# Kernel optimization log

Hardware: AMD Instinct MI355X
Metric: run time of the kernel (lower is better)

Reference implementation:

```python
import jax, jax.numpy as jnp
import numpy as np

B, H, W, C = 8, 64, 64, 256
CK = C // 8  # key/query dim of conv_f / conv_g


def setup_inputs() -> dict:
    key = jax.random.key(0)
    ks = jax.random.split(key, 10)
    s = lambda fan_in: 1.0 / np.sqrt(fan_in)
    return {
        "x": jax.random.normal(ks[0], (B, H, W, C), dtype=jnp.float32),
        "Wf": jax.random.normal(ks[1], (C, CK), dtype=jnp.float32) * s(C),
        "bf": jnp.zeros((CK,), dtype=jnp.float32),
        "Wg": jax.random.normal(ks[2], (C, CK), dtype=jnp.float32) * s(C),
        "bg": jnp.zeros((CK,), dtype=jnp.float32),
        "Wh": jax.random.normal(ks[3], (C, C), dtype=jnp.float32) * s(C),
        "bh": jnp.zeros((C,), dtype=jnp.float32),
        "Wo": jax.random.normal(ks[4], (C, C), dtype=jnp.float32) * s(C),
        "bo": jnp.zeros((C,), dtype=jnp.float32),
        # original init is zeros; use a random scalar so output/grads are nontrivial
        "gamma": jax.random.normal(ks[5], (1,), dtype=jnp.float32),
    }


def reference(x, Wf, bf, Wg, bg, Wh, bh, Wo, bo, gamma):
    b, h, w, c = x.shape
    n = h * w
    xf = x.reshape(b, n, c)                       # flatten spatial: [B, N, C]
    # 1x1 convs == per-pixel matmuls
    f = xf @ Wf + bf                              # [B, N, C//8]
    g = xf @ Wg + bg                              # [B, N, C//8]
    hh = xf @ Wh + bh                             # [B, N, C]
    # scores[b, i, j] = <g_i, f_j>; softmax over j (keys)
    scores = jnp.einsum("bnd,bmd->bnm", g, f)     # [B, N, N]
    attn = jax.nn.softmax(scores, axis=-1)
    o = jnp.einsum("bnm,bmc->bnc", attn, hh)      # [B, N, C]
    o = o @ Wo + bo                               # conv_o (1x1)
    out = gamma * o + xf                          # gamma residual
    return out.reshape(b, h, w, c)
```

## Files before the change

### kernel.cpp

```cpp
#include <hip/hip_runtime.h>
#include <hip/hip_fp16.h>
#include <hip/hip_bf16.h>

constexpr int BB  = 8;
constexpr int NN  = 4096;
constexpr int CC  = 256;
constexpr int CKK = 32;

typedef __attribute__((ext_vector_type(8))) short    short8;
typedef __attribute__((ext_vector_type(8))) _Float16 half8;
typedef __attribute__((ext_vector_type(4))) _Float16 half4;
typedef __attribute__((ext_vector_type(4))) float    f32x4;

__device__ __forceinline__ unsigned short bf16_bits(float v) {
    __hip_bfloat16 h = __float2bfloat16(v);
    return *reinterpret_cast<unsigned short*>(&h);
}
__device__ __forceinline__ float bf16_val(unsigned short u) {
    __hip_bfloat16 h = *reinterpret_cast<__hip_bfloat16*>(&u);
    return __bfloat162float(h);
}

__global__ __launch_bounds__(256) void prep_kernel(
    const float* __restrict__ Wf, const float* __restrict__ Wg,
    const float* __restrict__ Wh, const float* __restrict__ Wo,
    unsigned short* __restrict__ WThi, unsigned short* __restrict__ WTlo)
{
    const int n = blockIdx.x;
    const int k = threadIdx.x;
    float v;
    if      (n < 256) v = Wh[k * 256 + n];
    else if (n < 288) v = Wf[k * 32 + (n - 256)];
    else if (n < 320) v = Wg[k * 32 + (n - 288)];
    else              v = Wo[k * 256 + (n - 320)];
    const unsigned short hi = bf16_bits(v);
    WThi[n * 256 + k] = hi;
    WTlo[n * 256 + k] = bf16_bits(v - bf16_val(hi));
}

__global__ __launch_bounds__(256) void fgh_kernel(
    const float* __restrict__ x,
    const unsigned short* __restrict__ WThi, const unsigned short* __restrict__ WTlo,
    const float* __restrict__ bf, const float* __restrict__ bg,
    const float* __restrict__ bh,
    _Float16* __restrict__ fbuf, _Float16* __restrict__ gbuf,
    _Float16* __restrict__ hhT)
{
    const int tid = threadIdx.x, w = tid >> 6, lane = tid & 63;
    const int ln = lane & 15, lq = lane >> 4;
    const int px0 = blockIdx.x * 256 + w * 64;
    const int n0  = blockIdx.y * 64;

    f32x4 acc[4][4];
    #pragma unroll
    for (int i = 0; i < 4; ++i)
        #pragma unroll
        for (int j = 0; j < 4; ++j) acc[i][j] = {0.f, 0.f, 0.f, 0.f};

    float  rawA[4][8], rawB[4][8];
    short8 Ahi[4], Alo[4], Bhi[4], Blo[4];

    auto loadraw = [&](float (&rw)[4][8], int k0) {
        #pragma unroll
        for (int mt = 0; mt < 4; ++mt) {
            const float* xp = &x[(size_t)(px0 + mt * 16 + ln) * CC + k0 + lq * 8];
            *(float4*)&rw[mt][0] = *(const float4*)xp;
            *(float4*)&rw[mt][4] = *(const float4*)(xp + 4);
        }
    };
    auto loadB = [&](int k0) {
        #pragma unroll
        for (int nt = 0; nt < 4; ++nt) {
            const size_t boff = (size_t)(n0 + nt * 16 + ln) * 256 + k0 + lq * 8;
            Bhi[nt] = *(const short8*)&WThi[boff];
            Blo[nt] = *(const short8*)&WTlo[boff];
        }
    };
    auto convA = [&](float (&rw)[4][8]) {
        #pragma unroll
        for (int mt = 0; mt < 4; ++mt)
            #pragma unroll
            for (int j = 0; j < 8; ++j) {
                const unsigned short h = bf16_bits(rw[mt][j]);
                Ahi[mt][j] = (short)h;
                Alo[mt][j] = (short)bf16_bits(rw[mt][j] - bf16_val(h));
            }
    };
    auto mfmas = [&]() {
        #pragma unroll
        for (int nt = 0; nt < 4; ++nt)
            #pragma unroll
            for (int mt = 0; mt < 4; ++mt) {
                acc[mt][nt] = __builtin_amdgcn_mfma_f32_16x16x32_bf16(Ahi[mt], Bhi[nt], acc[mt][nt], 0, 0, 0);
                acc[mt][nt] = __builtin_amdgcn_mfma_f32_16x16x32_bf16(Ahi[mt], Blo[nt], acc[mt][nt], 0, 0, 0);
                acc[mt][nt] = __builtin_amdgcn_mfma_f32_16x16x32_bf16(Alo[mt], Bhi[nt], acc[mt][nt], 0, 0, 0);
            }
    };

    loadraw(rawA, 0);
    #pragma unroll 1
    for (int t = 0; t < 4; ++t) {
        const int k0 = t * 64;
        loadB(k0);
        loadraw(rawB, k0 + 32);
        convA(rawA);
        mfmas();
        loadB(k0 + 32);
        loadraw(rawA, (k0 + 64) & 255);
        convA(rawB);
        mfmas();
    }

    const int b = px0 >> 12;
    if (blockIdx.y < 4) {
        #pragma unroll
        for (int nt = 0; nt < 4; ++nt) {
            const int c = n0 + nt * 16 + ln;
            const float bias = bh[c];
            #pragma unroll
            for (int mt = 0; mt < 4; ++mt) {
                half4 hv;
                #pragma unroll
                for (int r = 0; r < 4; ++r) hv[r] = (_Float16)(acc[mt][nt][r] + bias);
                const int npix = (px0 & (NN - 1)) + mt * 16 + lq * 4;
                *(half4*)&hhT[((size_t)(b * CC + c)) * NN + npix] = hv;
            }
        }
    } else {
        #pragma unroll
        for (int nt = 0; nt < 4; ++nt) {
            const int d = (nt & 1) * 16 + ln;
            const float bias = (nt < 2) ? bf[d] : bg[d];
            _Float16* dst = (nt < 2) ? fbuf : gbuf;
            #pragma unroll
            for (int mt = 0; mt < 4; ++mt)
                #pragma unroll
                for (int r = 0; r < 4; ++r)
                    dst[(size_t)(px0 + mt * 16 + lq * 4 + r) * CKK + d] =
                        (_Float16)(acc[mt][nt][r] + bias);
        }
    }
}

__global__ __launch_bounds__(256, 2) void attn_kernel(
    const _Float16* __restrict__ fbuf, const _Float16* __restrict__ gbuf,
    const _Float16* __restrict__ hhT, float* __restrict__ obuf)
{
    __shared__ _Float16 P[2][64 * 72];
    __shared__ float mxbuf[4][64];
    __shared__ float rsbuf[4][64];

    const int tid = threadIdx.x, w = tid >> 6, lane = tid & 63;
    const int ln = lane & 15, lq = lane >> 4;
    const int b  = blockIdx.x & 7;
    const int q0 = (blockIdx.x >> 3) * 64;
    const int cb = w * 64;

    const f32x4 zero = {0.f, 0.f, 0.f, 0.f};
    constexpr float LOG2E = 1.4426950408889634f;

    half8 Bg[4];
    #pragma unroll
    for (int qt = 0; qt < 4; ++qt)
        Bg[qt] = *(const half8*)&gbuf[(size_t)(b * NN + q0 + qt * 16 + ln) * CKK + lq * 8];

    const _Float16* fb = &fbuf[(size_t)(b * NN + w * 16 + ln) * CKK + lq * 8];
    const _Float16* hb = &hhT[((size_t)(b * CC + cb + ln)) * NN + lq * 8];

    float mx[4];
    #pragma unroll
    for (int qt = 0; qt < 4; ++qt) mx[qt] = -1e30f;
    half8 Afc = *(const half8*)fb;
    #pragma unroll 1
    for (int j0 = 0; j0 < NN; j0 += 64) {
        const int jn = (j0 + 64 < NN) ? j0 + 64 : j0;
        const half8 Afn = *(const half8*)&fb[(size_t)jn * CKK];
        #pragma unroll
        for (int qt = 0; qt < 4; ++qt) {
            const f32x4 s = __builtin_amdgcn_mfma_f32_16x16x32_f16(Afc, Bg[qt], zero, 0, 0, 0);
            mx[qt] = fmaxf(mx[qt], fmaxf(fmaxf(s[0], s[1]), fmaxf(s[2], s[3])));
        }
        Afc = Afn;
    }
    #pragma unroll
    for (int qt = 0; qt < 4; ++qt) {
        mx[qt] = fmaxf(mx[qt], __shfl_xor(mx[qt], 16));
        mx[qt] = fmaxf(mx[qt], __shfl_xor(mx[qt], 32));
    }
    if (lane < 16) {
        #pragma unroll
        for (int qt = 0; qt < 4; ++qt) mxbuf[w][qt * 16 + ln] = mx[qt];
    }
    __syncthreads();
    float mk[4];
    #pragma unroll
    for (int qt = 0; qt < 4; ++qt)
        mk[qt] = LOG2E * fmaxf(fmaxf(mxbuf[0][qt * 16 + ln], mxbuf[1][qt * 16 + ln]),
                               fmaxf(mxbuf[2][qt * 16 + ln], mxbuf[3][qt * 16 + ln]));

    f32x4 O[4][4];
    #pragma unroll
    for (int qt = 0; qt < 4; ++qt)
        #pragma unroll
        for (int ct = 0; ct < 4; ++ct) O[qt][ct] = zero;
    float psum[4] = {0.f, 0.f, 0.f, 0.f};

    auto phaseA = [&](const half8& Af, _Float16* Pb) {
        #pragma unroll
        for (int qt = 0; qt < 4; ++qt) {
            const f32x4 s = __builtin_amdgcn_mfma_f32_16x16x32_f16(Af, Bg[qt], zero, 0, 0, 0);
            half4 ph;
            float ps = 0.f;
            #pragma unroll
            for (int r = 0; r < 4; ++r) {
                const float p = exp2f(fmaf(s[r], LOG2E, -mk[qt]));
                ps += p;
                ph[r] = (_Float16)p;
            }
            psum[qt] += ps;
            *(half4*)&Pb[(qt * 16 + ln) * 72 + w * 16 + lq * 4] = ph;
        }
    };

    auto loadBh = [&](half8 (&Bh)[4][2], int j0) {
        #pragma unroll
        for (int ct = 0; ct < 4; ++ct)
            #pragma unroll
            for (int kh = 0; kh < 2; ++kh)
                Bh[ct][kh] = *(const half8*)&hb[(size_t)ct * 16 * NN + j0 + kh * 32];
    };

    auto phaseB = [&](const half8 (&Bh)[4][2], const _Float16* Pb) {
        __builtin_amdgcn_s_setprio(1);
        #pragma unroll
        for (int qt = 0; qt < 4; ++qt) {
            const half8 Ap0 = *(const half8*)&Pb[(qt * 16 + ln) * 72 + lq * 8];
            const half8 Ap1 = *(const half8*)&Pb[(qt * 16 + ln) * 72 + 32 + lq * 8];
            #pragma unroll
            for (int ct = 0; ct < 4; ++ct) {
                O[qt][ct] = __builtin_amdgcn_mfma_f32_16x16x32_f16(Ap0, Bh[ct][0], O[qt][ct], 0, 0, 0);
                O[qt][ct] = __builtin_amdgcn_mfma_f32_16x16x32_f16(Ap1, Bh[ct][1], O[qt][ct], 0, 0, 0);
            }
        }
        __builtin_amdgcn_s_setprio(0);
    };

    half8 Bh0[4][2], Bh1[4][2];
    half8 Af0, Af1;
    loadBh(Bh0, 0);
    Af0 = *(const half8*)fb;

    #pragma unroll 1
    for (int j0 = 0; j0 < NN; j0 += 128) {
        phaseA(Af0, P[0]);
        __syncthreads();
        loadBh(Bh1, j0 + 64);
        Af1 = *(const half8*)&fb[(size_t)(j0 + 64) * CKK];
        phaseB(Bh0, P[0]);
        phaseA(Af1, P[1]);
        __syncthreads();
        if (j0 + 128 < NN) {
            loadBh(Bh0, j0 + 128);
            Af0 = *(const half8*)&fb[(size_t)(j0 + 128) * CKK];
        }
        phaseB(Bh1, P[1]);
    }

    #pragma unroll
    for (int qt = 0; qt < 4; ++qt) {
        psum[qt] += __shfl_xor(psum[qt], 16);
        psum[qt] += __shfl_xor(psum[qt], 32);
    }
    if (lane < 16) {
        #pragma unroll
        for (int qt = 0; qt < 4; ++qt) rsbuf[w][qt * 16 + ln] = psum[qt];
    }
    __syncthreads();

    #pragma unroll
    for (int qt = 0; qt < 4; ++qt)
        #pragma unroll
        for (int r = 0; r < 4; ++r) {
            const int q = qt * 16 + lq * 4 + r;
            const float rinv = 1.0f / (rsbuf[0][q] + rsbuf[1][q] + rsbuf[2][q] + rsbuf[3][q]);
            #pragma unroll
            for (int ct = 0; ct < 4; ++ct)
                obuf[((size_t)(b * NN + q0 + q)) * CC + cb + ct * 16 + ln] = O[qt][ct][r] * rinv;
        }
}

__global__ __launch_bounds__(256) void out_kernel(
    const float* __restrict__ obuf,
    const unsigned short* __restrict__ WThi, const unsigned short* __restrict__ WTlo,
    const float* __restrict__ bo, const float* __restrict__ gamma,
    const float* __restrict__ x, float* __restrict__ out)
{
    const int tid = threadIdx.x, w = tid >> 6, lane = tid & 63;
    const int ln = lane & 15, lq = lane >> 4;
    const int px0 = blockIdx.x * 256 + w * 64;
    const int n0  = blockIdx.y * 64;

    f32x4 acc[4][4];
    #pragma unroll
    for (int i = 0; i < 4; ++i)
        #pragma unroll
        for (int j = 0; j < 4; ++j) acc[i][j] = {0.f, 0.f, 0.f, 0.f};

    float  rawA[4][8], rawB[4][8];
    short8 Ahi[4], Alo[4], Bhi[4], Blo[4];

    auto loadraw = [&](float (&rw)[4][8], int k0) {
        #pragma unroll
        for (int mt = 0; mt < 4; ++mt) {
            const float* op = &obuf[(size_t)(px0 + mt * 16 + ln) * CC + k0 + lq * 8];
            *(float4*)&rw[mt][0] = *(const float4*)op;
            *(float4*)&rw[mt][4] = *(const float4*)(op + 4);
        }
    };
    auto loadB = [&](int k0) {
        #pragma unroll
        for (int nt = 0; nt < 4; ++nt) {
            const size_t boff = (size_t)(320 + n0 + nt * 16 + ln) * 256 + k0 + lq * 8;
            Bhi[nt] = *(const short8*)&WThi[boff];
            Blo[nt] = *(const short8*)&WTlo[boff];
        }
    };
    auto convA = [&](float (&rw)[4][8]) {
        #pragma unroll
        for (int mt = 0; mt < 4; ++mt)
            #pragma unroll
            for (int j = 0; j < 8; ++j) {
                const unsigned short h = bf16_bits(rw[mt][j]);
                Ahi[mt][j] = (short)h;
                Alo[mt][j] = (short)bf16_bits(rw[mt][j] - bf16_val(h));
            }
    };
    auto mfmas = [&]() {
        #pragma unroll
        for (int nt = 0; nt < 4; ++nt)
            #pragma unroll
            for (int mt = 0; mt < 4; ++mt) {
                acc[mt][nt] = __builtin_amdgcn_mfma_f32_16x16x32_bf16(Ahi[mt], Bhi[nt], acc[mt][nt], 0, 0, 0);
                acc[mt][nt] = __builtin_amdgcn_mfma_f32_16x16x32_bf16(Ahi[mt], Blo[nt], acc[mt][nt], 0, 0, 0);
                acc[mt][nt] = __builtin_amdgcn_mfma_f32_16x16x32_bf16(Alo[mt], Bhi[nt], acc[mt][nt], 0, 0, 0);
            }
    };

    loadraw(rawA, 0);
    #pragma unroll 1
    for (int t = 0; t < 4; ++t) {
        const int k0 = t * 64;
        loadB(k0);
        loadraw(rawB, k0 + 32);
        convA(rawA);
        mfmas();
        loadB(k0 + 32);
        loadraw(rawA, (k0 + 64) & 255);
        convA(rawB);
        mfmas();
    }

    const float gm = gamma[0];
    #pragma unroll
    for (int nt = 0; nt < 4; ++nt) {
        const int c = n0 + nt * 16 + ln;
        const float bias = bo[c];
        #pragma unroll
        for (int mt = 0; mt < 4; ++mt)
            #pragma unroll
            for (int r = 0; r < 4; ++r) {
                const size_t idx = (size_t)(px0 + mt * 16 + lq * 4 + r) * CC + c;
                out[idx] = gm * (acc[mt][nt][r] + bias) + x[idx];
            }
    }
}

extern "C" void kernel_launch(void* const* d_in, const int* in_sizes, int n_in,
                              void* d_out, int out_size, void* d_ws, size_t ws_size,
                              hipStream_t stream)
{
    (void)in_sizes; (void)n_in; (void)out_size; (void)ws_size;

    const float* x     = (const float*)d_in[0];
    const float* Wf    = (const float*)d_in[1];
    const float* bf    = (const float*)d_in[2];
    const float* Wg    = (const float*)d_in[3];
    const float* bg    = (const float*)d_in[4];
    const float* Wh    = (const float*)d_in[5];
    const float* bh    = (const float*)d_in[6];
    const float* Wo    = (const float*)d_in[7];
    const float* bo    = (const float*)d_in[8];
    const float* gamma = (const float*)d_in[9];
    float* out = (float*)d_out;

    _Float16* fbuf = (_Float16*)d_ws;
    _Float16* gbuf = fbuf + (size_t)BB * NN * CKK;
    _Float16* hhT  = gbuf + (size_t)BB * NN * CKK;
    float*    obuf = (float*)(hhT + (size_t)BB * CC * NN);
    unsigned short* WThi = (unsigned short*)(obuf + (size_t)BB * NN * CC);
    unsigned short* WTlo = WThi + (size_t)576 * 256;

    prep_kernel<<<576, 256, 0, stream>>>(Wf, Wg, Wh, Wo, WThi, WTlo);
    fgh_kernel<<<dim3(BB * NN / 256, 5), 256, 0, stream>>>(x, WThi, WTlo, bf, bg, bh,
                                                           fbuf, gbuf, hhT);
    attn_kernel<<<BB * NN / 64, 256, 0, stream>>>(fbuf, gbuf, hhT, obuf);
    out_kernel<<<dim3(BB * NN / 256, 4), 256, 0, stream>>>(obuf, WThi, WTlo, bo, gamma, x, out);
}
```

Measured before the change: 324.8 us.

## Use 8 waves per attention block, splitting channels 32 per wave

The attention kernel moves from 4 to 8 waves per block. Each wave now computes scores for 16 of 128 keys per step and accumulates output for 32 channels instead of 64, which halves the O accumulators and doubles the key tile per step. Because of the fewer registers, the hh-operand prefetch no longer needs a double buffer; the single buffer is reloaded after each phaseB. The trade-off is less load/compute overlap and heavier LDS and barrier traffic across 8 waves.

New measurement: 329.5 us. About the same (+1.4%).

```diff
diff --git a/kernel.cpp b/kernel.cpp
--- a/kernel.cpp
+++ b/kernel.cpp
@@ -142,19 +142,19 @@
     }
 }
 
-__global__ __launch_bounds__(256, 2) void attn_kernel(
+__global__ __launch_bounds__(512) void attn_kernel(
     const _Float16* __restrict__ fbuf, const _Float16* __restrict__ gbuf,
     const _Float16* __restrict__ hhT, float* __restrict__ obuf)
 {
-    __shared__ _Float16 P[2][64 * 72];
-    __shared__ float mxbuf[4][64];
-    __shared__ float rsbuf[4][64];
+    __shared__ _Float16 P[2][64 * 136];
+    __shared__ float mxbuf[8][64];
+    __shared__ float rsbuf[8][64];
 
     const int tid = threadIdx.x, w = tid >> 6, lane = tid & 63;
     const int ln = lane & 15, lq = lane >> 4;
     const int b  = blockIdx.x & 7;
     const int q0 = (blockIdx.x >> 3) * 64;
-    const int cb = w * 64;
+    const int cb = w * 32;
 
     const f32x4 zero = {0.f, 0.f, 0.f, 0.f};
     constexpr float LOG2E = 1.4426950408889634f;
@@ -172,8 +172,8 @@
     for (int qt = 0; qt < 4; ++qt) mx[qt] = -1e30f;
     half8 Afc = *(const half8*)fb;
     #pragma unroll 1
-    for (int j0 = 0; j0 < NN; j0 += 64) {
-        const int jn = (j0 + 64 < NN) ? j0 + 64 : j0;
+    for (int j0 = 0; j0 < NN; j0 += 128) {
+        const int jn = (j0 + 128 < NN) ? j0 + 128 : j0;
         const half8 Afn = *(const half8*)&fb[(size_t)jn * CKK];
         #pragma unroll
         for (int qt = 0; qt < 4; ++qt) {
@@ -194,15 +194,18 @@
     __syncthreads();
     float mk[4];
     #pragma unroll
+    for (int qt = 0; qt < 4; ++qt) {
+        float m = mxbuf[0][qt * 16 + ln];
+        #pragma unroll
+        for (int ww = 1; ww < 8; ++ww) m = fmaxf(m, mxbuf[ww][qt * 16 + ln]);
+        mk[qt] = LOG2E * m;
+    }
+
+    f32x4 O[4][2];
+    #pragma unroll
     for (int qt = 0; qt < 4; ++qt)
-        mk[qt] = LOG2E * fmaxf(fmaxf(mxbuf[0][qt * 16 + ln], mxbuf[1][qt * 16 + ln]),
-                               fmaxf(mxbuf[2][qt * 16 + ln], mxbuf[3][qt * 16 + ln]));
-
-    f32x4 O[4][4];
-    #pragma unroll
-    for (int qt = 0; qt < 4; ++qt)
-        #pragma unroll
-        for (int ct = 0; ct < 4; ++ct) O[qt][ct] = zero;
+        #pragma unroll
+        for (int ct = 0; ct < 2; ++ct) O[qt][ct] = zero;
     float psum[4] = {0.f, 0.f, 0.f, 0.f};
 
     auto phaseA = [&](const half8& Af, _Float16* Pb) {
@@ -218,52 +221,49 @@
                 ph[r] = (_Float16)p;
             }
             psum[qt] += ps;
-            *(half4*)&Pb[(qt * 16 + ln) * 72 + w * 16 + lq * 4] = ph;
-        }
-    };
-
-    auto loadBh = [&](half8 (&Bh)[4][2], int j0) {
-        #pragma unroll
-        for (int ct = 0; ct < 4; ++ct)
-            #pragma unroll
-            for (int kh = 0; kh < 2; ++kh)
+            *(half4*)&Pb[(qt * 16 + ln) * 136 + w * 16 + lq * 4] = ph;
+        }
+    };
+
+    half8 Bh[2][4];
+    auto loadBh = [&](int j0) {
+        #pragma unroll
+        for (int ct = 0; ct < 2; ++ct)
+            #pragma unroll
+            for (int kh = 0; kh < 4; ++kh)
                 Bh[ct][kh] = *(const half8*)&hb[(size_t)ct * 16 * NN + j0 + kh * 32];
     };
 
-    auto phaseB = [&](const half8 (&Bh)[4][2], const _Float16* Pb) {
+    auto phaseB = [&](const _Float16* Pb) {
         __builtin_amdgcn_s_setprio(1);
         #pragma unroll
         for (int qt = 0; qt < 4; ++qt) {
-            const half8 Ap0 = *(const half8*)&Pb[(qt * 16 + ln) * 72 + lq * 8];
-            const half8 Ap1 = *(const half8*)&Pb[(qt * 16 + ln) * 72 + 32 + lq * 8];
-            #pragma unroll
-            for (int ct = 0; ct < 4; ++ct) {
-                O[qt][ct] = __builtin_amdgcn_mfma_f32_16x16x32_f16(Ap0, Bh[ct][0], O[qt][ct], 0, 0, 0);
-                O[qt][ct] = __builtin_amdgcn_mfma_f32_16x16x32_f16(Ap1, Bh[ct][1], O[qt][ct], 0, 0, 0);
+            #pragma unroll
+            for (int kh = 0; kh < 4; ++kh) {
+                const half8 Ap = *(const half8*)&Pb[(qt * 16 + ln) * 136 + kh * 32 + lq * 8];
+                O[qt][0] = __builtin_amdgcn_mfma_f32_16x16x32_f16(Ap, Bh[0][kh], O[qt][0], 0, 0, 0);
+                O[qt][1] = __builtin_amdgcn_mfma_f32_16x16x32_f16(Ap, Bh[1][kh], O[qt][1], 0, 0, 0);
             }
         }
         __builtin_amdgcn_s_setprio(0);
     };
 
-    half8 Bh0[4][2], Bh1[4][2];
-    half8 Af0, Af1;
-    loadBh(Bh0, 0);
-    Af0 = *(const half8*)fb;
+    half8 Af0 = *(const half8*)fb;
+    half8 Af1;
+    loadBh(0);
 
     #pragma unroll 1
-    for (int j0 = 0; j0 < NN; j0 += 128) {
+    for (int j0 = 0; j0 < NN; j0 += 256) {
         phaseA(Af0, P[0]);
         __syncthreads();
-        loadBh(Bh1, j0 + 64);
-        Af1 = *(const half8*)&fb[(size_t)(j0 + 64) * CKK];
-        phaseB(Bh0, P[0]);
+        Af1 = *(const half8*)&fb[(size_t)(j0 + 128) * CKK];
+        phaseB(P[0]);
+        loadBh(j0 + 128);
         phaseA(Af1, P[1]);
         __syncthreads();
-        if (j0 + 128 < NN) {
-            loadBh(Bh0, j0 + 128);
-            Af0 = *(const half8*)&fb[(size_t)(j0 + 128) * CKK];
-        }
-        phaseB(Bh1, P[1]);
+        Af0 = *(const half8*)&fb[(size_t)((j0 + 256) & (NN - 1)) * CKK];
+        phaseB(P[1]);
+        loadBh((j0 + 256) & (NN - 1));
     }
 
     #pragma unroll
@@ -282,9 +282,12 @@
         #pragma unroll
         for (int r = 0; r < 4; ++r) {
             const int q = qt * 16 + lq * 4 + r;
-            const float rinv = 1.0f / (rsbuf[0][q] + rsbuf[1][q] + rsbuf[2][q] + rsbuf[3][q]);
-            #pragma unroll
-            for (int ct = 0; ct < 4; ++ct)
+            float rs = rsbuf[0][q];
+            #pragma unroll
+            for (int ww = 1; ww < 8; ++ww) rs += rsbuf[ww][q];
+            const float rinv = 1.0f / rs;
+            #pragma unroll
+            for (int ct = 0; ct < 2; ++ct)
                 obuf[((size_t)(b * NN + q0 + q)) * CC + cb + ct * 16 + ln] = O[qt][ct][r] * rinv;
         }
 }
@@ -403,6 +406,6 @@
     prep_kernel<<<576, 256, 0, stream>>>(Wf, Wg, Wh, Wo, WThi, WTlo);
     fgh_kernel<<<dim3(BB * NN / 256, 5), 256, 0, stream>>>(x, WThi, WTlo, bf, bg, bh,
                                                            fbuf, gbuf, hhT);
-    attn_kernel<<<BB * NN / 64, 256, 0, stream>>>(fbuf, gbuf, hhT, obuf);
+    attn_kernel<<<BB * NN / 64, 512, 0, stream>>>(fbuf, gbuf, hhT, obuf);
     out_kernel<<<dim3(BB * NN / 256, 4), 256, 0, stream>>>(obuf, WThi, WTlo, bo, gamma, x, out);
 }
```

## Fuse output projection and residual into attention kernel epilogue via LDS

Applied to the files above, without the earlier changes.

The attention kernel now writes its normalized output tile into shared memory and immediately applies the conv_o projection (split-bf16 MFMA), bias, gamma scaling and residual add, removing the separate out_kernel. This eliminates the fp32 obuf round trip through global memory and one kernel launch. In exchange, shared memory per block grows substantially, which may limit occupancy, and the epilogue GEMM loads weights without prefetching.

Result: faster. 306.4 us (-5.7%).

```diff
diff --git a/kernel.cpp b/kernel.cpp
--- a/kernel.cpp
+++ b/kernel.cpp
@@ -144,9 +144,14 @@
 
 __global__ __launch_bounds__(256, 2) void attn_kernel(
     const _Float16* __restrict__ fbuf, const _Float16* __restrict__ gbuf,
-    const _Float16* __restrict__ hhT, float* __restrict__ obuf)
+    const _Float16* __restrict__ hhT,
+    const unsigned short* __restrict__ WThi, const unsigned short* __restrict__ WTlo,
+    const float* __restrict__ bo, const float* __restrict__ gamma,
+    const float* __restrict__ x, float* __restrict__ out)
 {
-    __shared__ _Float16 P[2][64 * 72];
+    __shared__ __align__(16) float OF[64 * 268];
+    _Float16* P0 = (_Float16*)OF;
+    _Float16* P1 = P0 + 64 * 72;
     __shared__ float mxbuf[4][64];
     __shared__ float rsbuf[4][64];
 
@@ -252,18 +257,18 @@
 
     #pragma unroll 1
     for (int j0 = 0; j0 < NN; j0 += 128) {
-        phaseA(Af0, P[0]);
+        phaseA(Af0, P0);
         __syncthreads();
         loadBh(Bh1, j0 + 64);
         Af1 = *(const half8*)&fb[(size_t)(j0 + 64) * CKK];
-        phaseB(Bh0, P[0]);
-        phaseA(Af1, P[1]);
+        phaseB(Bh0, P0);
+        phaseA(Af1, P1);
         __syncthreads();
         if (j0 + 128 < NN) {
             loadBh(Bh0, j0 + 128);
             Af0 = *(const half8*)&fb[(size_t)(j0 + 128) * CKK];
         }
-        phaseB(Bh1, P[1]);
+        phaseB(Bh1, P1);
     }
 
     #pragma unroll
@@ -285,93 +290,61 @@
             const float rinv = 1.0f / (rsbuf[0][q] + rsbuf[1][q] + rsbuf[2][q] + rsbuf[3][q]);
             #pragma unroll
             for (int ct = 0; ct < 4; ++ct)
-                obuf[((size_t)(b * NN + q0 + q)) * CC + cb + ct * 16 + ln] = O[qt][ct][r] * rinv;
-        }
-}
-
-__global__ __launch_bounds__(256) void out_kernel(
-    const float* __restrict__ obuf,
-    const unsigned short* __restrict__ WThi, const unsigned short* __restrict__ WTlo,
-    const float* __restrict__ bo, const float* __restrict__ gamma,
-    const float* __restrict__ x, float* __restrict__ out)
-{
-    const int tid = threadIdx.x, w = tid >> 6, lane = tid & 63;
-    const int ln = lane & 15, lq = lane >> 4;
-    const int px0 = blockIdx.x * 256 + w * 64;
-    const int n0  = blockIdx.y * 64;
-
-    f32x4 acc[4][4];
-    #pragma unroll
-    for (int i = 0; i < 4; ++i)
-        #pragma unroll
-        for (int j = 0; j < 4; ++j) acc[i][j] = {0.f, 0.f, 0.f, 0.f};
-
-    float  rawA[4][8], rawB[4][8];
-    short8 Ahi[4], Alo[4], Bhi[4], Blo[4];
-
-    auto loadraw = [&](float (&rw)[4][8], int k0) {
-        #pragma unroll
-        for (int mt = 0; mt < 4; ++mt) {
-            const float* op = &obuf[(size_t)(px0 + mt * 16 + ln) * CC + k0 + lq * 8];
-            *(float4*)&rw[mt][0] = *(const float4*)op;
-            *(float4*)&rw[mt][4] = *(const float4*)(op + 4);
-        }
-    };
-    auto loadB = [&](int k0) {
+                OF[q * 268 + cb + ct * 16 + ln] = O[qt][ct][r] * rinv;
+        }
+    __syncthreads();
+
+    {
+        const int n0 = w * 64;
+        f32x4 acc[4][4];
+        #pragma unroll
+        for (int i = 0; i < 4; ++i)
+            #pragma unroll
+            for (int j = 0; j < 4; ++j) acc[i][j] = {0.f, 0.f, 0.f, 0.f};
+
+        short8 Ahi[4], Alo[4];
+        #pragma unroll 1
+        for (int kc = 0; kc < 8; ++kc) {
+            const int k0 = kc * 32;
+            #pragma unroll
+            for (int mt = 0; mt < 4; ++mt) {
+                float av[8];
+                *(f32x4*)&av[0] = *(const f32x4*)&OF[(mt * 16 + ln) * 268 + k0 + lq * 8];
+                *(f32x4*)&av[4] = *(const f32x4*)&OF[(mt * 16 + ln) * 268 + k0 + lq * 8 + 4];
+                #pragma unroll
+                for (int j = 0; j < 8; ++j) {
+                    const unsigned short h = bf16_bits(av[j]);
+                    Ahi[mt][j] = (short)h;
+                    Alo[mt][j] = (short)bf16_bits(av[j] - bf16_val(h));
+                }
+            }
+            #pragma unroll
+            for (int nt = 0; nt < 4; ++nt) {
+                const size_t boff = (size_t)(320 + n0 + nt * 16 + ln) * 256 + k0 + lq * 8;
+                const short8 Bhi = *(const short8*)&WThi[boff];
+                const short8 Blo = *(const short8*)&WTlo[boff];
+                #pragma unroll
+                for (int mt = 0; mt < 4; ++mt) {
+                    acc[mt][nt] = __builtin_amdgcn_mfma_f32_16x16x32_bf16(Ahi[mt], Bhi, acc[mt][nt], 0, 0, 0);
+                    acc[mt][nt] = __builtin_amdgcn_mfma_f32_16x16x32_bf16(Ahi[mt], Blo, acc[mt][nt], 0, 0, 0);
+                    acc[mt][nt] = __builtin_amdgcn_mfma_f32_16x16x32_bf16(Alo[mt], Bhi, acc[mt][nt], 0, 0, 0);
+                }
+            }
+        }
+
+        const float gm = gamma[0];
         #pragma unroll
         for (int nt = 0; nt < 4; ++nt) {
-            const size_t boff = (size_t)(320 + n0 + nt * 16 + ln) * 256 + k0 + lq * 8;
-            Bhi[nt] = *(const short8*)&WThi[boff];
-            Blo[nt] = *(const short8*)&WTlo[boff];
-        }
-    };
-    auto convA = [&](float (&rw)[4][8]) {
-        #pragma unroll
-        for (int mt = 0; mt < 4; ++mt)
-            #pragma unroll
-            for (int j = 0; j < 8; ++j) {
-                const unsigned short h = bf16_bits(rw[mt][j]);
-                Ahi[mt][j] = (short)h;
-                Alo[mt][j] = (short)bf16_bits(rw[mt][j] - bf16_val(h));
-            }
-    };
-    auto mfmas = [&]() {
-        #pragma unroll
-        for (int nt = 0; nt < 4; ++nt)
-            #pragma unroll
-            for (int mt = 0; mt < 4; ++mt) {
-                acc[mt][nt] = __builtin_amdgcn_mfma_f32_16x16x32_bf16(Ahi[mt], Bhi[nt], acc[mt][nt], 0, 0, 0);
-                acc[mt][nt] = __builtin_amdgcn_mfma_f32_16x16x32_bf16(Ahi[mt], Blo[nt], acc[mt][nt], 0, 0, 0);
-                acc[mt][nt] = __builtin_amdgcn_mfma_f32_16x16x32_bf16(Alo[mt], Bhi[nt], acc[mt][nt], 0, 0, 0);
-            }
-    };
-
-    loadraw(rawA, 0);
-    #pragma unroll 1
-    for (int t = 0; t < 4; ++t) {
-        const int k0 = t * 64;
-        loadB(k0);
-        loadraw(rawB, k0 + 32);
-        convA(rawA);
-        mfmas();
-        loadB(k0 + 32);
-        loadraw(rawA, (k0 + 64) & 255);
-        convA(rawB);
-        mfmas();
-    }
-
-    const float gm = gamma[0];
-    #pragma unroll
-    for (int nt = 0; nt < 4; ++nt) {
-        const int c = n0 + nt * 16 + ln;
-        const float bias = bo[c];
-        #pragma unroll
-        for (int mt = 0; mt < 4; ++mt)
-            #pragma unroll
-            for (int r = 0; r < 4; ++r) {
-                const size_t idx = (size_t)(px0 + mt * 16 + lq * 4 + r) * CC + c;
-                out[idx] = gm * (acc[mt][nt][r] + bias) + x[idx];
-            }
+            const int c = n0 + nt * 16 + ln;
+            const float bias = bo[c];
+            #pragma unroll
+            for (int mt = 0; mt < 4; ++mt)
+                #pragma unroll
+                for (int r = 0; r < 4; ++r) {
+                    const size_t idx = (size_t)(b * NN + q0 + mt * 16 + lq * 4 + r) * CC + c;
+                    out[idx] = gm * (acc[mt][nt][r] + bias) + x[idx];
+                }
+        }
     }
 }
 
@@ -396,13 +369,12 @@
     _Float16* fbuf = (_Float16*)d_ws;
     _Float16* gbuf = fbuf + (size_t)BB * NN * CKK;
     _Float16* hhT  = gbuf + (size_t)BB * NN * CKK;
-    float*    obuf = (float*)(hhT + (size_t)BB * CC * NN);
-    unsigned short* WThi = (unsigned short*)(obuf + (size_t)BB * NN * CC);
+    unsigned short* WThi = (unsigned short*)(hhT + (size_t)BB * CC * NN);
     unsigned short* WTlo = WThi + (size_t)576 * 256;
 
     prep_kernel<<<576, 256, 0, stream>>>(Wf, Wg, Wh, Wo, WThi, WTlo);
     fgh_kernel<<<dim3(BB * NN / 256, 5), 256, 0, stream>>>(x, WThi, WTlo, bf, bg, bh,
                                                            fbuf, gbuf, hhT);
-    attn_kernel<<<BB * NN / 64, 256, 0, stream>>>(fbuf, gbuf, hhT, obuf);
-    out_kernel<<<dim3(BB * NN / 256, 4), 256, 0, stream>>>(obuf, WThi, WTlo, bo, gamma, x, out);
-}
+    attn_kernel<<<BB * NN / 64, 256, 0, stream>>>(fbuf, gbuf, hhT, WThi, WTlo,
+                                                  bo, gamma, x, out);
+}
```
